# Kernel tuning notes

Hardware: AMD Instinct MI355X
Metric: run time of the kernel (lower is better)

The kernel has to match this reference:

```python
import jax, jax.numpy as jnp
import numpy as np

DIM = 128
N = 8192
E = 262144
EPS = 1e-8  # torch.cosine_similarity eps


def setup_inputs() -> dict:
    key = jax.random.key(0)
    k1, k2, k3, k4 = jax.random.split(key, 4)
    x = jax.random.normal(k1, (N, DIM), dtype=jnp.float32)
    edge_index = jax.random.randint(k2, (2, E), 0, N, dtype=jnp.int32)
    # GCNConv parameters: linear weight (glorot-ish) and bias
    W_gcn = jax.random.normal(k3, (DIM, DIM), dtype=jnp.float32) / np.sqrt(DIM)
    b_gcn = jnp.zeros((DIM,), dtype=jnp.float32)
    return {"x": x, "edge_index": edge_index, "W_gcn": W_gcn, "b_gcn": b_gcn}


def _cosine_attention(x):
    # torch.cosine_similarity(x.unsqueeze(1), x.unsqueeze(0), dim=-1)
    # == (x @ x.T) / max(||x_i|| * ||x_j||, eps)
    nrm = jnp.sqrt(jnp.sum(x * x, axis=-1))                      # [N]
    denom = jnp.maximum(nrm[:, None] * nrm[None, :], EPS)        # [N, N]
    sim = (x @ x.T) / denom                                      # [N, N]
    return jax.nn.sigmoid(sim @ x)                               # [N, dim]


def _gcn_conv(x, edge_index, W, b):
    n = x.shape[0]
    xw = x @ W                                                   # [N, dim]
    # add self-loops
    loops = jnp.arange(n, dtype=edge_index.dtype)
    row = jnp.concatenate([edge_index[0], loops])                # source
    col = jnp.concatenate([edge_index[1], loops])                # target
    # symmetric normalization: deg computed on target nodes
    deg = jax.ops.segment_sum(jnp.ones_like(col, dtype=x.dtype), col, num_segments=n)
    dis = jnp.where(deg > 0, jax.lax.rsqrt(jnp.maximum(deg, 1.0)), 0.0)
    dis = jnp.where(deg > 0, deg ** -0.5, 0.0)
    norm = dis[row] * dis[col]                                   # [E+N]
    msgs = xw[row] * norm[:, None]                               # [E+N, dim]
    out = jax.ops.segment_sum(msgs, col, num_segments=n)         # [N, dim]
    return out + b


def reference(x, edge_index, W_gcn, b_gcn):
    att = _cosine_attention(x)
    g = _gcn_conv(x, edge_index, W_gcn, b_gcn)
    return g * att
```

## Files before the change

kernel.cpp:

```cpp
#include <hip/hip_runtime.h>
#include <math.h>

#define NN  8192
#define DIM 128
#define NE  262144
#define XB  128
#define HB  128
#define EPB (NE / HB)
#define EPT (EPB / 256)
#define RWB 32
#define BK  16

static __device__ __forceinline__ unsigned short f2bf(float f) {
  unsigned int u = __float_as_uint(f);
  return (unsigned short)((u + 0x7FFFu + ((u >> 16) & 1u)) >> 16);
}
static __device__ __forceinline__ float bf2f(unsigned short h) {
  return __uint_as_float((unsigned int)h << 16);
}

__global__ __launch_bounds__(256) void k_prep(const float* __restrict__ x,
    const int* __restrict__ ei, float* __restrict__ rinv,
    int* __restrict__ rank, int* __restrict__ partial,
    float* __restrict__ Mpart) {
  __shared__ float smem[64 * DIM + 64];
  int bid = blockIdx.x, tid = threadIdx.x;
  if (bid < XB) {
    float* xs  = smem;
    float* rvs = smem + 64 * DIM;
    int row0 = bid * 64;
    const float4* xsrc = (const float4*)(x + (size_t)row0 * DIM);
    float4* xdst = (float4*)xs;
    #pragma unroll
    for (int i = 0; i < 8; ++i) xdst[tid + 256 * i] = xsrc[tid + 256 * i];
    __syncthreads();
    int rr = tid >> 2, q = tid & 3;
    const float4* xr = (const float4*)&xs[rr * DIM + q * 32];
    float ss = 0.f;
    #pragma unroll
    for (int i = 0; i < 8; ++i) {
      float4 v = xr[i];
      ss += v.x * v.x + v.y * v.y + v.z * v.z + v.w * v.w;
    }
    ss += __shfl_xor(ss, 1);
    ss += __shfl_xor(ss, 2);
    if (q == 0) rvs[rr] = 1.0f / sqrtf(ss);
    __syncthreads();

    int ty = tid >> 4, tx = tid & 15;
    float acc[8][8];
    #pragma unroll
    for (int i = 0; i < 8; ++i)
      #pragma unroll
      for (int j = 0; j < 8; ++j) acc[i][j] = 0.f;

    #pragma unroll 2
    for (int r = 0; r < 64; ++r) {
      float4 a0 = *(const float4*)&xs[r * DIM + ty * 8];
      float4 a1 = *(const float4*)&xs[r * DIM + ty * 8 + 4];
      float4 b0 = *(const float4*)&xs[r * DIM + tx * 8];
      float4 b1 = *(const float4*)&xs[r * DIM + tx * 8 + 4];
      float rv = rvs[r];
      float a[8] = {a0.x * rv, a0.y * rv, a0.z * rv, a0.w * rv,
                    a1.x * rv, a1.y * rv, a1.z * rv, a1.w * rv};
      float b[8] = {b0.x, b0.y, b0.z, b0.w, b1.x, b1.y, b1.z, b1.w};
      #pragma unroll
      for (int i = 0; i < 8; ++i)
        #pragma unroll
        for (int j = 0; j < 8; ++j) acc[i][j] += a[i] * b[j];
    }
    float* o = Mpart + (size_t)bid * (DIM * DIM);
    #pragma unroll
    for (int i = 0; i < 8; ++i) {
      *(float4*)&o[(ty * 8 + i) * DIM + tx * 8]     = make_float4(acc[i][0], acc[i][1], acc[i][2], acc[i][3]);
      *(float4*)&o[(ty * 8 + i) * DIM + tx * 8 + 4] = make_float4(acc[i][4], acc[i][5], acc[i][6], acc[i][7]);
    }
  } else if (bid < XB + 2048) {
    int wave = tid >> 6, lane = tid & 63;
    int row  = (bid - XB) * 4 + wave;
    const float2* x2 = (const float2*)(x + (size_t)row * DIM);
    float2 v = x2[lane];
    float ss = v.x * v.x + v.y * v.y;
    #pragma unroll
    for (int m = 32; m; m >>= 1) ss += __shfl_xor(ss, m);
    if (lane == 0) rinv[row] = 1.0f / sqrtf(ss);
  } else {
    int h = bid - (XB + 2048);
    int* ldeg = (int*)smem;
    int4* lz = (int4*)ldeg;
    #pragma unroll
    for (int i = tid; i < NN / 4; i += 256) lz[i] = make_int4(0, 0, 0, 0);
    __syncthreads();
    int e0 = h * EPB + tid * EPT;
    int4 c0 = *(const int4*)(ei + NE + e0);
    int4 c1 = *(const int4*)(ei + NE + e0 + 4);
    int r0 = atomicAdd(&ldeg[c0.x], 1);
    int r1 = atomicAdd(&ldeg[c0.y], 1);
    int r2 = atomicAdd(&ldeg[c0.z], 1);
    int r3 = atomicAdd(&ldeg[c0.w], 1);
    int r4 = atomicAdd(&ldeg[c1.x], 1);
    int r5 = atomicAdd(&ldeg[c1.y], 1);
    int r6 = atomicAdd(&ldeg[c1.z], 1);
    int r7 = atomicAdd(&ldeg[c1.w], 1);
    *(int4*)(rank + e0)     = make_int4(r0, r1, r2, r3);
    *(int4*)(rank + e0 + 4) = make_int4(r4, r5, r6, r7);
    __syncthreads();
    #pragma unroll
    for (int i = tid * 4; i < NN; i += 1024)
      *(int4*)(partial + (size_t)h * NN + i) = *(int4*)&ldeg[i];
  }
}

__global__ __launch_bounds__(256) void k_mid(const float* __restrict__ Mpart,
    float* __restrict__ M, int* __restrict__ partial,
    int* __restrict__ deg, float* __restrict__ dis) {
  int bid = blockIdx.x, tid = threadIdx.x;
  if (bid < 64) {
    int j = bid * 256 + tid;
    float s = 0.f;
    #pragma unroll 4
    for (int k = 0; k < XB; ++k) s += Mpart[(size_t)k * (DIM * DIM) + j];
    M[j] = s;
  } else {
    int idx = (bid - 64) * 256 + tid;
    int4 run = make_int4(0, 0, 0, 0);
    #pragma unroll 4
    for (int b = 0; b < HB; ++b) {
      int4* p4 = (int4*)(partial + (size_t)b * NN);
      int4 v = p4[idx];
      p4[idx] = run;
      run.x += v.x; run.y += v.y; run.z += v.z; run.w += v.w;
    }
    int4 d = make_int4(run.x + 1, run.y + 1, run.z + 1, run.w + 1);
    *(int4*)(deg + idx * 4) = d;
    float4 ds;
    ds.x = rsqrtf((float)d.x); ds.y = rsqrtf((float)d.y);
    ds.z = rsqrtf((float)d.z); ds.w = rsqrtf((float)d.w);
    *(float4*)(dis + idx * 4) = ds;
  }
}

__global__ __launch_bounds__(1024) void k_scan(const int* __restrict__ deg,
    int* __restrict__ offs) {
  __shared__ int wsum[16];
  int t = threadIdx.x;
  int lane = t & 63, wave = t >> 6;
  int base_i = t * 8;
  int local[8], s = 0;
  int4 d0 = *(const int4*)(deg + base_i);
  int4 d1 = *(const int4*)(deg + base_i + 4);
  int cnt[8] = {d0.x - 1, d0.y - 1, d0.z - 1, d0.w - 1,
                d1.x - 1, d1.y - 1, d1.z - 1, d1.w - 1};
  #pragma unroll
  for (int j = 0; j < 8; ++j) { local[j] = s; s += cnt[j]; }
  int tot = s, sc = s;
  #pragma unroll
  for (int off = 1; off < 64; off <<= 1) {
    int v = __shfl_up(sc, off);
    if (lane >= off) sc += v;
  }
  if (lane == 63) wsum[wave] = sc;
  __syncthreads();
  if (wave == 0) {
    int v = (lane < 16) ? wsum[lane] : 0;
    #pragma unroll
    for (int off = 1; off < 16; off <<= 1) {
      int u = __shfl_up(v, off);
      if (lane >= off) v += u;
    }
    if (lane < 16) wsum[lane] = v;
  }
  __syncthreads();
  int base = (wave ? wsum[wave - 1] : 0) + sc - tot;
  #pragma unroll
  for (int j = 0; j < 8; ++j) offs[base_i + j] = base + local[j];
}

__global__ __launch_bounds__(256) void k_main(const float* __restrict__ x,
    const float* __restrict__ W, const float* __restrict__ M,
    const float* __restrict__ rinv, const float* __restrict__ dis,
    const int* __restrict__ ei, const int* __restrict__ offs,
    const int* __restrict__ partial, const int* __restrict__ rank,
    int* __restrict__ sorted, unsigned short* __restrict__ xws,
    float* __restrict__ att) {
  __shared__ float xs[RWB * DIM];
  __shared__ float Wl[BK * DIM];
  __shared__ float Ml[BK * DIM];
  __shared__ float rvs[RWB], dss[RWB];
  int bid = blockIdx.x, tid = threadIdx.x;
  if (bid < NN / RWB) {
    int row0 = bid * RWB;
    const float4* xsrc = (const float4*)(x + (size_t)row0 * DIM);
    float4* xdst = (float4*)xs;
    #pragma unroll
    for (int i = 0; i < 4; ++i) xdst[tid + 256 * i] = xsrc[tid + 256 * i];
    if (tid < RWB) { rvs[tid] = rinv[row0 + tid]; dss[tid] = dis[row0 + tid]; }

    int ty = tid >> 5, tx = tid & 31;
    int r0 = ty * 4;
    float4 aw[4], am[4];
    #pragma unroll
    for (int j = 0; j < 4; ++j) { aw[j] = make_float4(0,0,0,0); am[j] = make_float4(0,0,0,0); }

    for (int kk = 0; kk < DIM; kk += BK) {
      __syncthreads();
      const float4* Ws = (const float4*)(W + (size_t)kk * DIM);
      const float4* Ms = (const float4*)(M + (size_t)kk * DIM);
      float4 w0s = Ws[tid], w1s = Ws[tid + 256];
      float4 m0s = Ms[tid], m1s = Ms[tid + 256];
      ((float4*)Wl)[tid]       = w0s;
      ((float4*)Wl)[tid + 256] = w1s;
      ((float4*)Ml)[tid]       = m0s;
      ((float4*)Ml)[tid + 256] = m1s;
      __syncthreads();
      #pragma unroll
      for (int k4 = 0; k4 < BK; k4 += 4) {
        float4 xf[4];
        #pragma unroll
        for (int j = 0; j < 4; ++j)
          xf[j] = *(const float4*)&xs[(r0 + j) * DIM + kk + k4];
        #pragma unroll
        for (int k = 0; k < 4; ++k) {
          float4 wv = *(const float4*)&Wl[(k4 + k) * DIM + tx * 4];
          float4 mv = *(const float4*)&Ml[(k4 + k) * DIM + tx * 4];
          #pragma unroll
          for (int j = 0; j < 4; ++j) {
            float xv = ((const float*)&xf[j])[k];
            aw[j].x += xv * wv.x; aw[j].y += xv * wv.y;
            aw[j].z += xv * wv.z; aw[j].w += xv * wv.w;
            am[j].x += xv * mv.x; am[j].y += xv * mv.y;
            am[j].z += xv * mv.z; am[j].w += xv * mv.w;
          }
        }
      }
    }

    #pragma unroll
    for (int j = 0; j < 4; ++j) {
      int row = row0 + r0 + j;
      float rv = rvs[r0 + j], ds = dss[r0 + j];
      size_t o = (size_t)row * DIM + tx * 4;
      ushort4 wb;
      wb.x = f2bf(aw[j].x * ds);
      wb.y = f2bf(aw[j].y * ds);
      wb.z = f2bf(aw[j].z * ds);
      wb.w = f2bf(aw[j].w * ds);
      *(ushort4*)&xws[o] = wb;
      float4 g;
      g.x = 1.0f / (1.0f + __expf(-am[j].x * rv));
      g.y = 1.0f / (1.0f + __expf(-am[j].y * rv));
      g.z = 1.0f / (1.0f + __expf(-am[j].z * rv));
      g.w = 1.0f / (1.0f + __expf(-am[j].w * rv));
      *(float4*)&att[o] = g;
    }
  } else {
    int pb = bid - NN / RWB;
    int e0 = pb * EPB + tid * EPT;
    int4 s0 = *(const int4*)(ei + e0);
    int4 s1 = *(const int4*)(ei + e0 + 4);
    int4 c0 = *(const int4*)(ei + NE + e0);
    int4 c1 = *(const int4*)(ei + NE + e0 + 4);
    int4 r0 = *(const int4*)(rank + e0);
    int4 r1 = *(const int4*)(rank + e0 + 4);
    const int* pfx = partial + (size_t)pb * NN;
    sorted[offs[c0.x] + pfx[c0.x] + r0.x] = s0.x;
    sorted[offs[c0.y] + pfx[c0.y] + r0.y] = s0.y;
    sorted[offs[c0.z] + pfx[c0.z] + r0.z] = s0.z;
    sorted[offs[c0.w] + pfx[c0.w] + r0.w] = s0.w;
    sorted[offs[c1.x] + pfx[c1.x] + r1.x] = s1.x;
    sorted[offs[c1.y] + pfx[c1.y] + r1.y] = s1.y;
    sorted[offs[c1.z] + pfx[c1.z] + r1.z] = s1.z;
    sorted[offs[c1.w] + pfx[c1.w] + r1.w] = s1.w;
  }
}

__global__ __launch_bounds__(128) void k_gather(const int* __restrict__ sorted,
    const int* __restrict__ offs, const int* __restrict__ deg,
    const float* __restrict__ dis, const unsigned short* __restrict__ xws,
    const float* __restrict__ att, const float* __restrict__ bias,
    float* __restrict__ out) {
  int c = blockIdx.x, t = threadIdx.x;
  int base = offs[c];
  int cnt  = deg[c] - 1;
  float acc = bf2f(xws[(size_t)c * DIM + t]);
  int k = 0;
  for (; k + 4 <= cnt; k += 4) {
    int s0 = sorted[base + k + 0];
    int s1 = sorted[base + k + 1];
    int s2 = sorted[base + k + 2];
    int s3 = sorted[base + k + 3];
    float v0 = bf2f(xws[(size_t)s0 * DIM + t]);
    float v1 = bf2f(xws[(size_t)s1 * DIM + t]);
    float v2 = bf2f(xws[(size_t)s2 * DIM + t]);
    float v3 = bf2f(xws[(size_t)s3 * DIM + t]);
    acc += v0 + v1 + v2 + v3;
  }
  for (; k < cnt; ++k)
    acc += bf2f(xws[(size_t)sorted[base + k] * DIM + t]);
  float g = acc * dis[c] + bias[t];
  out[(size_t)c * DIM + t] = g * att[(size_t)c * DIM + t];
}

extern "C" void kernel_launch(void* const* d_in, const int* in_sizes, int n_in,
                              void* d_out, int out_size, void* d_ws, size_t ws_size,
                              hipStream_t stream) {
  const float* x  = (const float*)d_in[0];
  const int*   ei = (const int*)  d_in[1];
  const float* W  = (const float*)d_in[2];
  const float* b  = (const float*)d_in[3];
  float* out = (float*)d_out;

  unsigned short* xws = (unsigned short*)d_ws;
  float* att     = (float*)(xws + (size_t)NN * DIM);
  float* Mpart   = att + (size_t)NN * DIM;
  float* M       = Mpart + (size_t)XB * DIM * DIM;
  float* rinv    = M + DIM * DIM;
  float* dis     = rinv + NN;
  int*   deg     = (int*)(dis + NN);
  int*   offs    = deg + NN;
  int*   rank    = offs + NN;
  int*   partial = rank + NE;
  int*   sorted  = partial + (size_t)HB * NN;

  k_prep   <<<XB + 2048 + HB, 256, 0, stream>>>(x, ei, rinv, rank, partial, Mpart);
  k_mid    <<<72, 256, 0, stream>>>(Mpart, M, partial, deg, dis);
  k_scan   <<<1, 1024, 0, stream>>>(deg, offs);
  k_main   <<<NN / RWB + HB, 256, 0, stream>>>(x, W, M, rinv, dis, ei, offs,
                                               partial, rank, sorted, xws, att);
  k_gather <<<NN, 128, 0, stream>>>(sorted, offs, deg, dis, xws, att, b, out);
}
```

Baseline: 119.7 us.

## Fuse pipeline into one cooperative persistent kernel with grid syncs

```diff
diff --git a/kernel.cpp b/kernel.cpp
--- a/kernel.cpp
+++ b/kernel.cpp
@@ -1,15 +1,18 @@
 #include <hip/hip_runtime.h>
+#include <hip/hip_cooperative_groups.h>
 #include <math.h>
 
-#define NN  8192
-#define DIM 128
-#define NE  262144
-#define XB  128
-#define HB  128
-#define EPB (NE / HB)
-#define EPT (EPB / 256)
-#define RWB 32
-#define BK  16
+namespace cg = cooperative_groups;
+
+#define NN   8192
+#define DIM  128
+#define NE   262144
+#define XB   128
+#define HB   256
+#define EPB  (NE / HB)
+#define RWB  32
+#define BK   16
+#define SMEMF (64 * DIM + 64)
 
 static __device__ __forceinline__ unsigned short f2bf(float f) {
   unsigned int u = __float_as_uint(f);
@@ -19,141 +22,113 @@
   return __uint_as_float((unsigned int)h << 16);
 }
 
-__global__ __launch_bounds__(256) void k_prep(const float* __restrict__ x,
-    const int* __restrict__ ei, float* __restrict__ rinv,
-    int* __restrict__ rank, int* __restrict__ partial,
+
+static __device__ void ph_xtx(int u, int tid, float* smem,
+    const float* __restrict__ x, float* __restrict__ rinv,
     float* __restrict__ Mpart) {
-  __shared__ float smem[64 * DIM + 64];
-  int bid = blockIdx.x, tid = threadIdx.x;
-  if (bid < XB) {
-    float* xs  = smem;
-    float* rvs = smem + 64 * DIM;
-    int row0 = bid * 64;
-    const float4* xsrc = (const float4*)(x + (size_t)row0 * DIM);
-    float4* xdst = (float4*)xs;
+  float* xs  = smem;
+  float* rvs = smem + 64 * DIM;
+  int row0 = u * 64;
+  const float4* xsrc = (const float4*)(x + (size_t)row0 * DIM);
+  float4* xdst = (float4*)xs;
+  #pragma unroll
+  for (int i = 0; i < 8; ++i) xdst[tid + 256 * i] = xsrc[tid + 256 * i];
+  __syncthreads();
+  int rr = tid >> 2, q = tid & 3;
+  const float4* xr = (const float4*)&xs[rr * DIM + q * 32];
+  float ss = 0.f;
+  #pragma unroll
+  for (int i = 0; i < 8; ++i) {
+    float4 v = xr[i];
+    ss += v.x * v.x + v.y * v.y + v.z * v.z + v.w * v.w;
+  }
+  ss += __shfl_xor(ss, 1);
+  ss += __shfl_xor(ss, 2);
+  if (q == 0) { float rv = 1.0f / sqrtf(ss); rvs[rr] = rv; rinv[row0 + rr] = rv; }
+  __syncthreads();
+
+  int ty = tid >> 4, tx = tid & 15;
+  float acc[8][8];
+  #pragma unroll
+  for (int i = 0; i < 8; ++i)
     #pragma unroll
-    for (int i = 0; i < 8; ++i) xdst[tid + 256 * i] = xsrc[tid + 256 * i];
-    __syncthreads();
-    int rr = tid >> 2, q = tid & 3;
-    const float4* xr = (const float4*)&xs[rr * DIM + q * 32];
-    float ss = 0.f;
-    #pragma unroll
-    for (int i = 0; i < 8; ++i) {
-      float4 v = xr[i];
-      ss += v.x * v.x + v.y * v.y + v.z * v.z + v.w * v.w;
-    }
-    ss += __shfl_xor(ss, 1);
-    ss += __shfl_xor(ss, 2);
-    if (q == 0) rvs[rr] = 1.0f / sqrtf(ss);
-    __syncthreads();
-
-    int ty = tid >> 4, tx = tid & 15;
-    float acc[8][8];
+    for (int j = 0; j < 8; ++j) acc[i][j] = 0.f;
+  #pragma unroll 2
+  for (int r = 0; r < 64; ++r) {
+    float4 a0 = *(const float4*)&xs[r * DIM + ty * 8];
+    float4 a1 = *(const float4*)&xs[r * DIM + ty * 8 + 4];
+    float4 b0 = *(const float4*)&xs[r * DIM + tx * 8];
+    float4 b1 = *(const float4*)&xs[r * DIM + tx * 8 + 4];
+    float rv = rvs[r];
+    float a[8] = {a0.x * rv, a0.y * rv, a0.z * rv, a0.w * rv,
+                  a1.x * rv, a1.y * rv, a1.z * rv, a1.w * rv};
+    float b[8] = {b0.x, b0.y, b0.z, b0.w, b1.x, b1.y, b1.z, b1.w};
     #pragma unroll
     for (int i = 0; i < 8; ++i)
       #pragma unroll
-      for (int j = 0; j < 8; ++j) acc[i][j] = 0.f;
-
-    #pragma unroll 2
-    for (int r = 0; r < 64; ++r) {
-      float4 a0 = *(const float4*)&xs[r * DIM + ty * 8];
-      float4 a1 = *(const float4*)&xs[r * DIM + ty * 8 + 4];
-      float4 b0 = *(const float4*)&xs[r * DIM + tx * 8];
-      float4 b1 = *(const float4*)&xs[r * DIM + tx * 8 + 4];
-      float rv = rvs[r];
-      float a[8] = {a0.x * rv, a0.y * rv, a0.z * rv, a0.w * rv,
-                    a1.x * rv, a1.y * rv, a1.z * rv, a1.w * rv};
-      float b[8] = {b0.x, b0.y, b0.z, b0.w, b1.x, b1.y, b1.z, b1.w};
-      #pragma unroll
-      for (int i = 0; i < 8; ++i)
-        #pragma unroll
-        for (int j = 0; j < 8; ++j) acc[i][j] += a[i] * b[j];
-    }
-    float* o = Mpart + (size_t)bid * (DIM * DIM);
-    #pragma unroll
-    for (int i = 0; i < 8; ++i) {
-      *(float4*)&o[(ty * 8 + i) * DIM + tx * 8]     = make_float4(acc[i][0], acc[i][1], acc[i][2], acc[i][3]);
-      *(float4*)&o[(ty * 8 + i) * DIM + tx * 8 + 4] = make_float4(acc[i][4], acc[i][5], acc[i][6], acc[i][7]);
-    }
-  } else if (bid < XB + 2048) {
-    int wave = tid >> 6, lane = tid & 63;
-    int row  = (bid - XB) * 4 + wave;
-    const float2* x2 = (const float2*)(x + (size_t)row * DIM);
-    float2 v = x2[lane];
-    float ss = v.x * v.x + v.y * v.y;
-    #pragma unroll
-    for (int m = 32; m; m >>= 1) ss += __shfl_xor(ss, m);
-    if (lane == 0) rinv[row] = 1.0f / sqrtf(ss);
-  } else {
-    int h = bid - (XB + 2048);
-    int* ldeg = (int*)smem;
-    int4* lz = (int4*)ldeg;
-    #pragma unroll
-    for (int i = tid; i < NN / 4; i += 256) lz[i] = make_int4(0, 0, 0, 0);
-    __syncthreads();
-    int e0 = h * EPB + tid * EPT;
-    int4 c0 = *(const int4*)(ei + NE + e0);
-    int4 c1 = *(const int4*)(ei + NE + e0 + 4);
-    int r0 = atomicAdd(&ldeg[c0.x], 1);
-    int r1 = atomicAdd(&ldeg[c0.y], 1);
-    int r2 = atomicAdd(&ldeg[c0.z], 1);
-    int r3 = atomicAdd(&ldeg[c0.w], 1);
-    int r4 = atomicAdd(&ldeg[c1.x], 1);
-    int r5 = atomicAdd(&ldeg[c1.y], 1);
-    int r6 = atomicAdd(&ldeg[c1.z], 1);
-    int r7 = atomicAdd(&ldeg[c1.w], 1);
-    *(int4*)(rank + e0)     = make_int4(r0, r1, r2, r3);
-    *(int4*)(rank + e0 + 4) = make_int4(r4, r5, r6, r7);
-    __syncthreads();
-    #pragma unroll
-    for (int i = tid * 4; i < NN; i += 1024)
-      *(int4*)(partial + (size_t)h * NN + i) = *(int4*)&ldeg[i];
-  }
-}
-
-__global__ __launch_bounds__(256) void k_mid(const float* __restrict__ Mpart,
-    float* __restrict__ M, int* __restrict__ partial,
-    int* __restrict__ deg, float* __restrict__ dis) {
-  int bid = blockIdx.x, tid = threadIdx.x;
-  if (bid < 64) {
-    int j = bid * 256 + tid;
-    float s = 0.f;
-    #pragma unroll 4
-    for (int k = 0; k < XB; ++k) s += Mpart[(size_t)k * (DIM * DIM) + j];
-    M[j] = s;
-  } else {
-    int idx = (bid - 64) * 256 + tid;
-    int4 run = make_int4(0, 0, 0, 0);
-    #pragma unroll 4
-    for (int b = 0; b < HB; ++b) {
-      int4* p4 = (int4*)(partial + (size_t)b * NN);
-      int4 v = p4[idx];
-      p4[idx] = run;
-      run.x += v.x; run.y += v.y; run.z += v.z; run.w += v.w;
-    }
-    int4 d = make_int4(run.x + 1, run.y + 1, run.z + 1, run.w + 1);
-    *(int4*)(deg + idx * 4) = d;
-    float4 ds;
-    ds.x = rsqrtf((float)d.x); ds.y = rsqrtf((float)d.y);
-    ds.z = rsqrtf((float)d.z); ds.w = rsqrtf((float)d.w);
-    *(float4*)(dis + idx * 4) = ds;
-  }
-}
-
-__global__ __launch_bounds__(1024) void k_scan(const int* __restrict__ deg,
-    int* __restrict__ offs) {
-  __shared__ int wsum[16];
-  int t = threadIdx.x;
-  int lane = t & 63, wave = t >> 6;
-  int base_i = t * 8;
-  int local[8], s = 0;
-  int4 d0 = *(const int4*)(deg + base_i);
-  int4 d1 = *(const int4*)(deg + base_i + 4);
-  int cnt[8] = {d0.x - 1, d0.y - 1, d0.z - 1, d0.w - 1,
-                d1.x - 1, d1.y - 1, d1.z - 1, d1.w - 1};
-  #pragma unroll
-  for (int j = 0; j < 8; ++j) { local[j] = s; s += cnt[j]; }
-  int tot = s, sc = s;
+      for (int j = 0; j < 8; ++j) acc[i][j] += a[i] * b[j];
+  }
+  float* o = Mpart + (size_t)u * (DIM * DIM);
+  #pragma unroll
+  for (int i = 0; i < 8; ++i) {
+    *(float4*)&o[(ty * 8 + i) * DIM + tx * 8]     = make_float4(acc[i][0], acc[i][1], acc[i][2], acc[i][3]);
+    *(float4*)&o[(ty * 8 + i) * DIM + tx * 8 + 4] = make_float4(acc[i][4], acc[i][5], acc[i][6], acc[i][7]);
+  }
+}
+
+static __device__ void ph_hist(int h, int tid, int* ldeg,
+    const int* __restrict__ ei, int* __restrict__ gcnt, int* __restrict__ slot) {
+  int4* lz = (int4*)ldeg;
+  #pragma unroll
+  for (int i = tid; i < NN / 4; i += 256) lz[i] = make_int4(0, 0, 0, 0);
+  __syncthreads();
+  int e0 = h * EPB + tid * 4;
+  int4 c = *(const int4*)(ei + NE + e0);
+  int r0 = atomicAdd(&ldeg[c.x], 1);
+  int r1 = atomicAdd(&ldeg[c.y], 1);
+  int r2 = atomicAdd(&ldeg[c.z], 1);
+  int r3 = atomicAdd(&ldeg[c.w], 1);
+  __syncthreads();
+  int binb = tid * 32;
+  #pragma unroll
+  for (int i = 0; i < 8; ++i) {
+    int4 v = *(int4*)&ldeg[binb + i * 4];
+    if (v.x) ldeg[binb + i * 4 + 0] = atomicAdd(&gcnt[binb + i * 4 + 0], v.x);
+    if (v.y) ldeg[binb + i * 4 + 1] = atomicAdd(&gcnt[binb + i * 4 + 1], v.y);
+    if (v.z) ldeg[binb + i * 4 + 2] = atomicAdd(&gcnt[binb + i * 4 + 2], v.z);
+    if (v.w) ldeg[binb + i * 4 + 3] = atomicAdd(&gcnt[binb + i * 4 + 3], v.w);
+  }
+  __syncthreads();
+  int4 sl;
+  sl.x = ldeg[c.x] + r0;
+  sl.y = ldeg[c.y] + r1;
+  sl.z = ldeg[c.z] + r2;
+  sl.w = ldeg[c.w] + r3;
+  *(int4*)(slot + e0) = sl;
+}
+
+static __device__ void ph_mred(int u, int tid, float* smem,
+    const float* __restrict__ Mpart, float* __restrict__ Mmat) {
+  int j0 = u * 64;
+  int jj = tid & 63, sub = tid >> 6;
+  const float* mp = Mpart + (size_t)(sub * 32) * (DIM * DIM) + j0;
+  float s = 0.f;
+  #pragma unroll 4
+  for (int k = 0; k < 32; ++k) s += mp[(size_t)k * (DIM * DIM) + jj];
+  smem[sub * 64 + jj] = s;
+  __syncthreads();
+  if (tid < 64)
+    Mmat[j0 + tid] = smem[tid] + smem[64 + tid] + smem[128 + tid] + smem[192 + tid];
+}
+
+static __device__ void ph_scan(int tid, int* wsum,
+    const int* __restrict__ gcnt, int* __restrict__ offs, float* __restrict__ dis) {
+  int lane = tid & 63, wave = tid >> 6;
+  const int4* g4 = (const int4*)gcnt;
+  int s = 0;
+  #pragma unroll
+  for (int i = 0; i < 8; ++i) { int4 v = g4[tid * 8 + i]; s += v.x + v.y + v.z + v.w; }
+  int sc = s;
   #pragma unroll
   for (int off = 1; off < 64; off <<= 1) {
     int v = __shfl_up(sc, off);
@@ -161,127 +136,130 @@
   }
   if (lane == 63) wsum[wave] = sc;
   __syncthreads();
-  if (wave == 0) {
-    int v = (lane < 16) ? wsum[lane] : 0;
+  if (wave == 0 && lane < 4) {
+    int v = wsum[lane];
     #pragma unroll
-    for (int off = 1; off < 16; off <<= 1) {
+    for (int off = 1; off < 4; off <<= 1) {
       int u = __shfl_up(v, off);
       if (lane >= off) v += u;
     }
-    if (lane < 16) wsum[lane] = v;
-  }
-  __syncthreads();
-  int base = (wave ? wsum[wave - 1] : 0) + sc - tot;
-  #pragma unroll
-  for (int j = 0; j < 8; ++j) offs[base_i + j] = base + local[j];
-}
-
-__global__ __launch_bounds__(256) void k_main(const float* __restrict__ x,
-    const float* __restrict__ W, const float* __restrict__ M,
-    const float* __restrict__ rinv, const float* __restrict__ dis,
-    const int* __restrict__ ei, const int* __restrict__ offs,
-    const int* __restrict__ partial, const int* __restrict__ rank,
-    int* __restrict__ sorted, unsigned short* __restrict__ xws,
+    wsum[lane] = v;
+  }
+  __syncthreads();
+  int run = (wave ? wsum[wave - 1] : 0) + sc - s;
+  #pragma unroll
+  for (int i = 0; i < 8; ++i) {
+    int4 v = g4[tid * 8 + i];
+    int4 o;
+    o.x = run; run += v.x;
+    o.y = run; run += v.y;
+    o.z = run; run += v.z;
+    o.w = run; run += v.w;
+    *(int4*)&offs[tid * 32 + i * 4] = o;
+    float4 d;
+    d.x = rsqrtf((float)(v.x + 1)); d.y = rsqrtf((float)(v.y + 1));
+    d.z = rsqrtf((float)(v.z + 1)); d.w = rsqrtf((float)(v.w + 1));
+    *(float4*)&dis[tid * 32 + i * 4] = d;
+  }
+}
+
+static __device__ void ph_gemm(int u, int tid, float* smem,
+    const float* __restrict__ x, const float* __restrict__ W,
+    const float* __restrict__ Mmat, const float* __restrict__ rinv,
+    const float* __restrict__ dis, unsigned short* __restrict__ xws,
     float* __restrict__ att) {
-  __shared__ float xs[RWB * DIM];
-  __shared__ float Wl[BK * DIM];
-  __shared__ float Ml[BK * DIM];
-  __shared__ float rvs[RWB], dss[RWB];
-  int bid = blockIdx.x, tid = threadIdx.x;
-  if (bid < NN / RWB) {
-    int row0 = bid * RWB;
-    const float4* xsrc = (const float4*)(x + (size_t)row0 * DIM);
-    float4* xdst = (float4*)xs;
+  float* xs  = smem;
+  float* Wl  = smem + 4096;
+  float* Ml  = smem + 6144;
+  float* rvs = smem + 8192;
+  float* dss = smem + 8224;
+  int row0 = u * RWB;
+  const float4* xsrc = (const float4*)(x + (size_t)row0 * DIM);
+  float4* xdst = (float4*)xs;
+  #pragma unroll
+  for (int i = 0; i < 4; ++i) xdst[tid + 256 * i] = xsrc[tid + 256 * i];
+  if (tid < RWB) { rvs[tid] = rinv[row0 + tid]; dss[tid] = dis[row0 + tid]; }
+
+  int ty = tid >> 5, tx = tid & 31;
+  int r0 = ty * 4;
+  float4 aw[4], am[4];
+  #pragma unroll
+  for (int j = 0; j < 4; ++j) { aw[j] = make_float4(0,0,0,0); am[j] = make_float4(0,0,0,0); }
+
+  for (int kk = 0; kk < DIM; kk += BK) {
+    __syncthreads();
+    const float4* Ws = (const float4*)(W + (size_t)kk * DIM);
+    const float4* Ms = (const float4*)(Mmat + (size_t)kk * DIM);
+    float4 w0s = Ws[tid], w1s = Ws[tid + 256];
+    float4 m0s = Ms[tid], m1s = Ms[tid + 256];
+    ((float4*)Wl)[tid]       = w0s;
+    ((float4*)Wl)[tid + 256] = w1s;
+    ((float4*)Ml)[tid]       = m0s;
+    ((float4*)Ml)[tid + 256] = m1s;
+    __syncthreads();
     #pragma unroll
-    for (int i = 0; i < 4; ++i) xdst[tid + 256 * i] = xsrc[tid + 256 * i];
-    if (tid < RWB) { rvs[tid] = rinv[row0 + tid]; dss[tid] = dis[row0 + tid]; }
-
-    int ty = tid >> 5, tx = tid & 31;
-    int r0 = ty * 4;
-    float4 aw[4], am[4];
-    #pragma unroll
-    for (int j = 0; j < 4; ++j) { aw[j] = make_float4(0,0,0,0); am[j] = make_float4(0,0,0,0); }
-
-    for (int kk = 0; kk < DIM; kk += BK) {
-      __syncthreads();
-      const float4* Ws = (const float4*)(W + (size_t)kk * DIM);
-      const float4* Ms = (const float4*)(M + (size_t)kk * DIM);
-      float4 w0s = Ws[tid], w1s = Ws[tid + 256];
-      float4 m0s = Ms[tid], m1s = Ms[tid + 256];
-      ((float4*)Wl)[tid]       = w0s;
-      ((float4*)Wl)[tid + 256] = w1s;
-      ((float4*)Ml)[tid]       = m0s;
-      ((float4*)Ml)[tid + 256] = m1s;
-      __syncthreads();
+    for (int k4 = 0; k4 < BK; k4 += 4) {
+      float4 xf[4];
       #pragma unroll
-      for (int k4 = 0; k4 < BK; k4 += 4) {
-        float4 xf[4];
+      for (int j = 0; j < 4; ++j)
+        xf[j] = *(const float4*)&xs[(r0 + j) * DIM + kk + k4];
+      #pragma unroll
+      for (int k = 0; k < 4; ++k) {
+        float4 wv = *(const float4*)&Wl[(k4 + k) * DIM + tx * 4];
+        float4 mv = *(const float4*)&Ml[(k4 + k) * DIM + tx * 4];
         #pragma unroll
-        for (int j = 0; j < 4; ++j)
-          xf[j] = *(const float4*)&xs[(r0 + j) * DIM + kk + k4];
-        #pragma unroll
-        for (int k = 0; k < 4; ++k) {
-          float4 wv = *(const float4*)&Wl[(k4 + k) * DIM + tx * 4];
-          float4 mv = *(const float4*)&Ml[(k4 + k) * DIM + tx * 4];
-          #pragma unroll
-          for (int j = 0; j < 4; ++j) {
-            float xv = ((const float*)&xf[j])[k];
-            aw[j].x += xv * wv.x; aw[j].y += xv * wv.y;
-            aw[j].z += xv * wv.z; aw[j].w += xv * wv.w;
-            am[j].x += xv * mv.x; am[j].y += xv * mv.y;
-            am[j].z += xv * mv.z; am[j].w += xv * mv.w;
-          }
+        for (int j = 0; j < 4; ++j) {
+          float xv = ((const float*)&xf[j])[k];
+          aw[j].x += xv * wv.x; aw[j].y += xv * wv.y;
+          aw[j].z += xv * wv.z; aw[j].w += xv * wv.w;
+          am[j].x += xv * mv.x; am[j].y += xv * mv.y;
+          am[j].z += xv * mv.z; am[j].w += xv * mv.w;
         }
       }
     }
-
-    #pragma unroll
-    for (int j = 0; j < 4; ++j) {
-      int row = row0 + r0 + j;
-      float rv = rvs[r0 + j], ds = dss[r0 + j];
-      size_t o = (size_t)row * DIM + tx * 4;
-      ushort4 wb;
-      wb.x = f2bf(aw[j].x * ds);
-      wb.y = f2bf(aw[j].y * ds);
-      wb.z = f2bf(aw[j].z * ds);
-      wb.w = f2bf(aw[j].w * ds);
-      *(ushort4*)&xws[o] = wb;
-      float4 g;
-      g.x = 1.0f / (1.0f + __expf(-am[j].x * rv));
-      g.y = 1.0f / (1.0f + __expf(-am[j].y * rv));
-      g.z = 1.0f / (1.0f + __expf(-am[j].z * rv));
-      g.w = 1.0f / (1.0f + __expf(-am[j].w * rv));
-      *(float4*)&att[o] = g;
-    }
-  } else {
-    int pb = bid - NN / RWB;
-    int e0 = pb * EPB + tid * EPT;
-    int4 s0 = *(const int4*)(ei + e0);
-    int4 s1 = *(const int4*)(ei + e0 + 4);
-    int4 c0 = *(const int4*)(ei + NE + e0);
-    int4 c1 = *(const int4*)(ei + NE + e0 + 4);
-    int4 r0 = *(const int4*)(rank + e0);
-    int4 r1 = *(const int4*)(rank + e0 + 4);
-    const int* pfx = partial + (size_t)pb * NN;
-    sorted[offs[c0.x] + pfx[c0.x] + r0.x] = s0.x;
-    sorted[offs[c0.y] + pfx[c0.y] + r0.y] = s0.y;
-    sorted[offs[c0.z] + pfx[c0.z] + r0.z] = s0.z;
-    sorted[offs[c0.w] + pfx[c0.w] + r0.w] = s0.w;
-    sorted[offs[c1.x] + pfx[c1.x] + r1.x] = s1.x;
-    sorted[offs[c1.y] + pfx[c1.y] + r1.y] = s1.y;
-    sorted[offs[c1.z] + pfx[c1.z] + r1.z] = s1.z;
-    sorted[offs[c1.w] + pfx[c1.w] + r1.w] = s1.w;
-  }
-}
-
-__global__ __launch_bounds__(128) void k_gather(const int* __restrict__ sorted,
-    const int* __restrict__ offs, const int* __restrict__ deg,
+  }
+  #pragma unroll
+  for (int j = 0; j < 4; ++j) {
+    int row = row0 + r0 + j;
+    float rv = rvs[r0 + j], ds = dss[r0 + j];
+    size_t o = (size_t)row * DIM + tx * 4;
+    ushort4 wb;
+    wb.x = f2bf(aw[j].x * ds);
+    wb.y = f2bf(aw[j].y * ds);
+    wb.z = f2bf(aw[j].z * ds);
+    wb.w = f2bf(aw[j].w * ds);
+    *(ushort4*)&xws[o] = wb;
+    float4 g;
+    g.x = 1.0f / (1.0f + __expf(-am[j].x * rv));
+    g.y = 1.0f / (1.0f + __expf(-am[j].y * rv));
+    g.z = 1.0f / (1.0f + __expf(-am[j].z * rv));
+    g.w = 1.0f / (1.0f + __expf(-am[j].w * rv));
+    *(float4*)&att[o] = g;
+  }
+}
+
+static __device__ void ph_place(int u, int tid,
+    const int* __restrict__ ei, const int* __restrict__ offs,
+    const int* __restrict__ slot, int* __restrict__ sorted) {
+  int e0 = u * EPB + tid * 4;
+  int4 sv = *(const int4*)(ei + e0);
+  int4 cv = *(const int4*)(ei + NE + e0);
+  int4 sl = *(const int4*)(slot + e0);
+  sorted[offs[cv.x] + sl.x] = sv.x;
+  sorted[offs[cv.y] + sl.y] = sv.y;
+  sorted[offs[cv.z] + sl.z] = sv.z;
+  sorted[offs[cv.w] + sl.w] = sv.w;
+}
+
+static __device__ void ph_gather(int u, int tid,
+    const int* __restrict__ offs, const int* __restrict__ gcnt,
     const float* __restrict__ dis, const unsigned short* __restrict__ xws,
     const float* __restrict__ att, const float* __restrict__ bias,
-    float* __restrict__ out) {
-  int c = blockIdx.x, t = threadIdx.x;
+    const int* __restrict__ sorted, float* __restrict__ out) {
+  int sub = tid >> 7, t = tid & 127;
+  int c = u * 2 + sub;
   int base = offs[c];
-  int cnt  = deg[c] - 1;
+  int cnt  = gcnt[c];
   float acc = bf2f(xws[(size_t)c * DIM + t]);
   int k = 0;
   for (; k + 4 <= cnt; k += 4) {
@@ -301,6 +279,76 @@
   out[(size_t)c * DIM + t] = g * att[(size_t)c * DIM + t];
 }
 
+__global__ __launch_bounds__(256, 2) void k_all(
+    const float* __restrict__ x, const int* __restrict__ ei,
+    const float* __restrict__ W, const float* __restrict__ bias,
+    float* __restrict__ out,
+    unsigned short* __restrict__ xws, float* __restrict__ att,
+    float* __restrict__ Mpart, float* __restrict__ Mmat,
+    float* __restrict__ rinv, float* __restrict__ dis,
+    int* __restrict__ gcnt, int* __restrict__ offs,
+    int* __restrict__ slot, int* __restrict__ sorted) {
+  cg::grid_group grid = cg::this_grid();
+  __shared__ float smem[SMEMF];
+  int bid = blockIdx.x, tid = threadIdx.x, G = gridDim.x;
+
+  for (int u = bid; u < XB + HB; u += G) {
+    if (u < XB) ph_xtx(u, tid, smem, x, rinv, Mpart);
+    else        ph_hist(u - XB, tid, (int*)smem, ei, gcnt, slot);
+    __syncthreads();
+  }
+  grid.sync();
+  for (int u = bid; u < 257; u += G) {
+    if (u < 256) ph_mred(u, tid, smem, Mpart, Mmat);
+    else         ph_scan(tid, (int*)smem, gcnt, offs, dis);
+    __syncthreads();
+  }
+  grid.sync();
+  for (int u = bid; u < NN / RWB + HB; u += G) {
+    if (u < NN / RWB) ph_gemm(u, tid, smem, x, W, Mmat, rinv, dis, xws, att);
+    else              ph_place(u - NN / RWB, tid, ei, offs, slot, sorted);
+    __syncthreads();
+  }
+  grid.sync();
+  for (int u = bid; u < NN / 2; u += G)
+    ph_gather(u, tid, offs, gcnt, dis, xws, att, bias, sorted, out);
+}
+
+__global__ __launch_bounds__(256, 2) void k_pA(const float* __restrict__ x,
+    const int* __restrict__ ei, float* __restrict__ rinv,
+    float* __restrict__ Mpart, int* __restrict__ gcnt, int* __restrict__ slot) {
+  __shared__ float smem[SMEMF];
+  int u = blockIdx.x, tid = threadIdx.x;
+  if (u < XB) ph_xtx(u, tid, smem, x, rinv, Mpart);
+  else        ph_hist(u - XB, tid, (int*)smem, ei, gcnt, slot);
+}
+__global__ __launch_bounds__(256, 2) void k_pB(const float* __restrict__ Mpart,
+    float* __restrict__ Mmat, const int* __restrict__ gcnt,
+    int* __restrict__ offs, float* __restrict__ dis) {
+  __shared__ float smem[SMEMF];
+  int u = blockIdx.x, tid = threadIdx.x;
+  if (u < 256) ph_mred(u, tid, smem, Mpart, Mmat);
+  else         ph_scan(tid, (int*)smem, gcnt, offs, dis);
+}
+__global__ __launch_bounds__(256, 2) void k_pC(const float* __restrict__ x,
+    const float* __restrict__ W, const float* __restrict__ Mmat,
+    const float* __restrict__ rinv, const float* __restrict__ dis,
+    const int* __restrict__ ei, const int* __restrict__ offs,
+    const int* __restrict__ slot, int* __restrict__ sorted,
+    unsigned short* __restrict__ xws, float* __restrict__ att) {
+  __shared__ float smem[SMEMF];
+  int u = blockIdx.x, tid = threadIdx.x;
+  if (u < NN / RWB) ph_gemm(u, tid, smem, x, W, Mmat, rinv, dis, xws, att);
+  else              ph_place(u - NN / RWB, tid, ei, offs, slot, sorted);
+}
+__global__ __launch_bounds__(256, 2) void k_pD(const int* __restrict__ offs,
+    const int* __restrict__ gcnt, const float* __restrict__ dis,
+    const unsigned short* __restrict__ xws, const float* __restrict__ att,
+    const float* __restrict__ bias, const int* __restrict__ sorted,
+    float* __restrict__ out) {
+  ph_gather(blockIdx.x, threadIdx.x, offs, gcnt, dis, xws, att, bias, sorted, out);
+}
+
 extern "C" void kernel_launch(void* const* d_in, const int* in_sizes, int n_in,
                               void* d_out, int out_size, void* d_ws, size_t ws_size,
                               hipStream_t stream) {
@@ -311,21 +359,33 @@
   float* out = (float*)d_out;
 
   unsigned short* xws = (unsigned short*)d_ws;
-  float* att     = (float*)(xws + (size_t)NN * DIM);
-  float* Mpart   = att + (size_t)NN * DIM;
-  float* M       = Mpart + (size_t)XB * DIM * DIM;
-  float* rinv    = M + DIM * DIM;
-  float* dis     = rinv + NN;
-  int*   deg     = (int*)(dis + NN);
-  int*   offs    = deg + NN;
-  int*   rank    = offs + NN;
-  int*   partial = rank + NE;
-  int*   sorted  = partial + (size_t)HB * NN;
-
-  k_prep   <<<XB + 2048 + HB, 256, 0, stream>>>(x, ei, rinv, rank, partial, Mpart);
-  k_mid    <<<72, 256, 0, stream>>>(Mpart, M, partial, deg, dis);
-  k_scan   <<<1, 1024, 0, stream>>>(deg, offs);
-  k_main   <<<NN / RWB + HB, 256, 0, stream>>>(x, W, M, rinv, dis, ei, offs,
-                                               partial, rank, sorted, xws, att);
-  k_gather <<<NN, 128, 0, stream>>>(sorted, offs, deg, dis, xws, att, b, out);
-}
+  float* att   = (float*)(xws + (size_t)NN * DIM);
+  float* Mpart = att + (size_t)NN * DIM;
+  float* Mmat  = Mpart + (size_t)XB * DIM * DIM;
+  float* rinv  = Mmat + DIM * DIM;
+  float* dis   = rinv + NN;
+  int*   gcnt  = (int*)(dis + NN);
+  int*   offs  = gcnt + NN;
+  int*   slot  = offs + NN;
+  int*   sorted= slot + NE;
+
+  hipMemsetAsync(gcnt, 0, NN * sizeof(int), stream);
+
+  void* args[] = {(void*)&x, (void*)&ei, (void*)&W, (void*)&b, (void*)&out,
+                  (void*)&xws, (void*)&att, (void*)&Mpart, (void*)&Mmat,
+                  (void*)&rinv, (void*)&dis, (void*)&gcnt, (void*)&offs,
+                  (void*)&slot, (void*)&sorted};
+  hipError_t e = hipLaunchCooperativeKernel((const void*)k_all, dim3(512),
+                                            dim3(256), args, 0, stream);
+  if (e != hipSuccess)
+    e = hipLaunchCooperativeKernel((const void*)k_all, dim3(256),
+                                   dim3(256), args, 0, stream);
+  if (e != hipSuccess) {
+    (void)hipGetLastError();
+    k_pA<<<XB + HB, 256, 0, stream>>>(x, ei, rinv, Mpart, gcnt, slot);
+    k_pB<<<257, 256, 0, stream>>>(Mpart, Mmat, gcnt, offs, dis);
+    k_pC<<<NN / RWB + HB, 256, 0, stream>>>(x, W, Mmat, rinv, dis, ei, offs,
+                                            slot, sorted, xws, att);
+    k_pD<<<NN / 2, 256, 0, stream>>>(offs, gcnt, dis, xws, att, b, sorted, out);
+  }
+}
```

New measurement: 321.3 us. +168.3%, slower.
